# Kernel tuning notes

Hardware: AMD Instinct MI355X
Metric: run time of the kernel (lower is better)

## Reference

```python
import jax, jax.numpy as jnp
import numpy as np

IN_FEATURES = 1024
NUM_EXPERTS = 64
TOP_K = 2


def setup_inputs() -> dict:
    key = jax.random.key(0)
    kx, kw, kb = jax.random.split(key, 3)
    x = jax.random.normal(kx, (8, 4096, IN_FEATURES), dtype=jnp.float32)
    # nn.Linear init scale ~ 1/sqrt(in_features)
    bound = 1.0 / np.sqrt(IN_FEATURES)
    W = jax.random.uniform(kw, (NUM_EXPERTS, IN_FEATURES), dtype=jnp.float32, minval=-bound, maxval=bound)
    b = jax.random.uniform(kb, (NUM_EXPERTS,), dtype=jnp.float32, minval=-bound, maxval=bound)
    return {"x": x, "W": W, "b": b}


def reference(x, W, b):
    # logits: [B, S, E]
    logits = jnp.einsum("bsd,ed->bse", x, W) + b
    gates = jax.nn.softmax(logits, axis=-1)
    top_k_gates, top_k_indices = jax.lax.top_k(gates, TOP_K)
    return top_k_gates, top_k_indices
```

## Files before the change

### kernel.cpp

```cpp
#include <hip/hip_runtime.h>

#define D 1024
#define E 64
#define TPB 256
#define TOKS 64
#define NCH 8
#define CHB 32768

typedef __attribute__((ext_vector_type(8))) short bf16x8;
typedef __attribute__((ext_vector_type(8))) unsigned short u16x8;
typedef __attribute__((ext_vector_type(4))) float f32x4;
typedef __attribute__((ext_vector_type(4))) unsigned int u32x4;

__device__ __forceinline__ unsigned short bf16_rne(float f) {
    unsigned u = __builtin_bit_cast(unsigned, f);
    u += 0x7fffu + ((u >> 16) & 1u);
    return (unsigned short)(u >> 16);
}
__device__ __forceinline__ float bf16_to_f(unsigned short h) {
    unsigned u = ((unsigned)h) << 16;
    return __builtin_bit_cast(float, u);
}
__device__ __forceinline__ unsigned cvt_pk_bf16(float a, float b) {
    unsigned r;
    asm("v_cvt_pk_bf16_f32 %0, %1, %2" : "=v"(r) : "v"(a), "v"(b));
    return r;
}
__device__ __forceinline__ float lo_val(unsigned p) {
    return __builtin_bit_cast(float, p << 16);
}
__device__ __forceinline__ float hi_val(unsigned p) {
    return __builtin_bit_cast(float, p & 0xffff0000u);
}

__device__ __forceinline__ void split8_rne(f32x4 a, f32x4 b, bf16x8& hv, bf16x8& lv) {
    unsigned h0 = cvt_pk_bf16(a[0], a[1]);
    unsigned h1 = cvt_pk_bf16(a[2], a[3]);
    unsigned h2 = cvt_pk_bf16(b[0], b[1]);
    unsigned h3 = cvt_pk_bf16(b[2], b[3]);
    unsigned l0 = cvt_pk_bf16(a[0] - lo_val(h0), a[1] - hi_val(h0));
    unsigned l1 = cvt_pk_bf16(a[2] - lo_val(h1), a[3] - hi_val(h1));
    unsigned l2 = cvt_pk_bf16(b[0] - lo_val(h2), b[1] - hi_val(h2));
    unsigned l3 = cvt_pk_bf16(b[2] - lo_val(h3), b[3] - hi_val(h3));
    hv = __builtin_bit_cast(bf16x8, (u32x4){h0, h1, h2, h3});
    lv = __builtin_bit_cast(bf16x8, (u32x4){l0, l1, l2, l3});
}

__global__ __launch_bounds__(256) void router_prep(
        const float* __restrict__ W, unsigned short* __restrict__ Ws) {
    int t = blockIdx.x * 256 + threadIdx.x;
    int lane = t & 63;
    int nt = (t >> 6) & 3;
    int ks = t >> 8;
    int n = lane & 15, q = lane >> 4;
    const float* src = W + (size_t)(nt * 16 + n) * D + ks * 32 + q * 8;
    u16x8 hv, lv;
#pragma unroll
    for (int j = 0; j < 8; ++j) {
        float v = src[j];
        unsigned short h = bf16_rne(v);
        hv[j] = h;
        lv[j] = bf16_rne(v - bf16_to_f(h));
    }
    size_t base = ((size_t)(ks * 8 + nt * 2) * 64 + lane) * 8;
    *(u16x8*)(Ws + base)          = hv;
    *(u16x8*)(Ws + base + 64 * 8) = lv;
}

__global__ __launch_bounds__(TPB) void router_main(
        const float* __restrict__ x, const unsigned short* __restrict__ Ws,
        const float* __restrict__ bias, float* __restrict__ out, int T) {
    __shared__ __align__(16) union SM {
        unsigned char buf[2][CHB];
        float ls[TOKS][E + 1];
    } sm;
    __shared__ float sbias[E];

    const int tid  = threadIdx.x;
    const int lane = tid & 63;
    const int wid  = tid >> 6;
    const int n    = lane & 15;
    const int q    = lane >> 4;
    const int t0   = blockIdx.x * TOKS;

    if (tid < E) sbias[tid] = bias[tid];

    const float* arow = x + (size_t)(t0 + wid * 16 + n) * D + q * 8;
    const u32x4* gws  = (const u32x4*)Ws;

    f32x4 c0 = {0.f, 0.f, 0.f, 0.f}, c1 = c0, c2 = c0, c3 = c0;

    u32x4 W0, W1, W2, W3, W4, W5, W6, W7;
    f32x4 A0u, A0v, A1u, A1v, A2u, A2v, A3u, A3v;
    f32x4 N0u, N0v, N1u, N1v, N2u, N2v, N3u, N3v;

#define ISSUEW(c_) do {                                               \
        const u32x4* _g = gws + (size_t)(c_) * 2048 + tid;            \
        W0 = _g[0];    W1 = _g[256];  W2 = _g[512];  W3 = _g[768];    \
        W4 = _g[1024]; W5 = _g[1280]; W6 = _g[1536]; W7 = _g[1792];   \
    } while (0)

#define WRITEW(bi_) do {                                              \
        u32x4* _l = (u32x4*)sm.buf[bi_] + tid;                        \
        _l[0]    = W0; _l[256]  = W1; _l[512]  = W2; _l[768]  = W3;   \
        _l[1024] = W4; _l[1280] = W5; _l[1536] = W6; _l[1792] = W7;   \
    } while (0)

#define ISSUEA(p0u,p0v,p1u,p1v,p2u,p2v,p3u,p3v, c_) do {              \
        const float* _b = arow + (size_t)(c_) * 128;                  \
        p0u = *(const f32x4*)(_b);       p0v = *(const f32x4*)(_b + 4);   \
        p1u = *(const f32x4*)(_b + 32);  p1v = *(const f32x4*)(_b + 36);  \
        p2u = *(const f32x4*)(_b + 64);  p2v = *(const f32x4*)(_b + 68);  \
        p3u = *(const f32x4*)(_b + 96);  p3v = *(const f32x4*)(_b + 100); \
    } while (0)

#define MFMA __builtin_amdgcn_mfma_f32_16x16x32_bf16
#define COMPSTEP(bi_, ksl_, au_, av_) do {                            \
        bf16x8 ah, al;                                                \
        split8_rne(au_, av_, ah, al);                                 \
        const char* _p = (const char*)sm.buf[bi_] + (ksl_) * 8192 + lane * 16; \
        {                                                             \
            bf16x8 bh = *(const bf16x8*)(_p);                         \
            bf16x8 bl = *(const bf16x8*)(_p + 1024);                  \
            c0 = MFMA(ah, bh, c0, 0, 0, 0);                           \
            c0 = MFMA(al, bh, c0, 0, 0, 0);                           \
            c0 = MFMA(ah, bl, c0, 0, 0, 0);                           \
        }                                                             \
        {                                                             \
            bf16x8 bh = *(const bf16x8*)(_p + 2048);                  \
            bf16x8 bl = *(const bf16x8*)(_p + 3072);                  \
            c1 = MFMA(ah, bh, c1, 0, 0, 0);                           \
            c1 = MFMA(al, bh, c1, 0, 0, 0);                           \
            c1 = MFMA(ah, bl, c1, 0, 0, 0);                           \
        }                                                             \
        {                                                             \
            bf16x8 bh = *(const bf16x8*)(_p + 4096);                  \
            bf16x8 bl = *(const bf16x8*)(_p + 5120);                  \
            c2 = MFMA(ah, bh, c2, 0, 0, 0);                           \
            c2 = MFMA(al, bh, c2, 0, 0, 0);                           \
            c2 = MFMA(ah, bl, c2, 0, 0, 0);                           \
        }                                                             \
        {                                                             \
            bf16x8 bh = *(const bf16x8*)(_p + 6144);                  \
            bf16x8 bl = *(const bf16x8*)(_p + 7168);                  \
            c3 = MFMA(ah, bh, c3, 0, 0, 0);                           \
            c3 = MFMA(al, bh, c3, 0, 0, 0);                           \
            c3 = MFMA(ah, bl, c3, 0, 0, 0);                           \
        }                                                             \
    } while (0)

#define COMPCHUNK(bi_, p0u,p0v,p1u,p1v,p2u,p2v,p3u,p3v) do {          \
        COMPSTEP(bi_, 0, p0u, p0v);                                   \
        COMPSTEP(bi_, 1, p1u, p1v);                                   \
        COMPSTEP(bi_, 2, p2u, p2v);                                   \
        COMPSTEP(bi_, 3, p3u, p3v);                                   \
    } while (0)

    ISSUEW(0);
    ISSUEA(A0u,A0v,A1u,A1v,A2u,A2v,A3u,A3v, 0);
    WRITEW(0);
    __syncthreads();

    for (int c = 0; c < NCH; c += 2) {
        ISSUEW(c + 1);
        ISSUEA(N0u,N0v,N1u,N1v,N2u,N2v,N3u,N3v, c + 1);
        COMPCHUNK(0, A0u,A0v,A1u,A1v,A2u,A2v,A3u,A3v);
        WRITEW(1);
        __syncthreads();
        ISSUEW((c + 2) & (NCH - 1));
        ISSUEA(A0u,A0v,A1u,A1v,A2u,A2v,A3u,A3v, (c + 2) & (NCH - 1));
        COMPCHUNK(1, N0u,N0v,N1u,N1v,N2u,N2v,N3u,N3v);
        WRITEW(0);
        __syncthreads();
    }

    {
        const int row = wid * 16 + q * 4;
#define STORE_C(c_, nt_) do {                                         \
            int col = (nt_) * 16 + n;                                 \
            float bv = sbias[col];                                    \
            sm.ls[row + 0][col] = c_[0] + bv;                         \
            sm.ls[row + 1][col] = c_[1] + bv;                         \
            sm.ls[row + 2][col] = c_[2] + bv;                         \
            sm.ls[row + 3][col] = c_[3] + bv;                         \
        } while (0)
        STORE_C(c0, 0); STORE_C(c1, 1); STORE_C(c2, 2); STORE_C(c3, 3);
#undef STORE_C
    }
    __syncthreads();

    if (tid < TOKS) {
        float m1 = -3.4e38f, m2 = -3.4e38f;
        int i1 = 0, i2 = 0;
        for (int e = 0; e < E; ++e) {
            float v = sm.ls[tid][e];
            if (v > m1) { m2 = m1; i2 = i1; m1 = v; i1 = e; }
            else if (v > m2) { m2 = v; i2 = e; }
        }
        float Z = 0.f;
        for (int e = 0; e < E; ++e) Z += __expf(sm.ls[tid][e] - m1);
        float inv = 1.f / Z;
        int gt = t0 + tid;
        out[(size_t)gt * 2]     = inv;
        out[(size_t)gt * 2 + 1] = __expf(m2 - m1) * inv;
        float* oi = out + (size_t)T * 2;
        oi[(size_t)gt * 2]     = (float)i1;
        oi[(size_t)gt * 2 + 1] = (float)i2;
    }
}

extern "C" void kernel_launch(void* const* d_in, const int* in_sizes, int n_in,
                              void* d_out, int out_size, void* d_ws, size_t ws_size,
                              hipStream_t stream) {
    const float* x = (const float*)d_in[0];
    const float* W = (const float*)d_in[1];
    const float* b = (const float*)d_in[2];
    float* out = (float*)d_out;
    unsigned short* Ws = (unsigned short*)d_ws;
    int T = in_sizes[0] / D;
    hipLaunchKernelGGL(router_prep, dim3(32), dim3(256), 0, stream, W, Ws);
    hipLaunchKernelGGL(router_main, dim3(T / TOKS), dim3(TPB), 0, stream,
                       x, Ws, b, out, T);
}
```

Before: 204.0 us.

## Stage activation tiles through LDS with coalesced loads and halve chunk size

Activations were read straight from global memory per MFMA lane with strided 32-byte pieces. They are now loaded by rows of 16 contiguous float4s per token into a padded shared-memory tile, double-buffered alongside the weights, and read back in fragment layout. The chunk size drops from 128 to 64 K-elements (16 chunks), which cuts registers and LDS per stage but doubles the number of barriers. The goal is more coalesced global reads of x and lower register pressure, at the cost of extra LDS traffic and synchronisation.

```diff
diff --git a/kernel.cpp b/kernel.cpp
--- a/kernel.cpp
+++ b/kernel.cpp
@@ -4,8 +4,9 @@
 #define E 64
 #define TPB 256
 #define TOKS 64
-#define NCH 8
-#define CHB 32768
+#define NCH 16
+#define WCB 16384
+#define APITCH 68
 
 typedef __attribute__((ext_vector_type(8))) short bf16x8;
 typedef __attribute__((ext_vector_type(8))) unsigned short u16x8;
@@ -71,7 +72,10 @@
         const float* __restrict__ x, const unsigned short* __restrict__ Ws,
         const float* __restrict__ bias, float* __restrict__ out, int T) {
     __shared__ __align__(16) union SM {
-        unsigned char buf[2][CHB];
+        struct {
+            unsigned char w[2][WCB];
+            float a[2][TOKS][APITCH];
+        } k;
         float ls[TOKS][E + 1];
     } sm;
     __shared__ float sbias[E];
@@ -82,43 +86,46 @@
     const int n    = lane & 15;
     const int q    = lane >> 4;
     const int t0   = blockIdx.x * TOKS;
+    const int arow = tid >> 4;
+    const int acol = (tid & 15) * 4;
 
     if (tid < E) sbias[tid] = bias[tid];
 
-    const float* arow = x + (size_t)(t0 + wid * 16 + n) * D + q * 8;
-    const u32x4* gws  = (const u32x4*)Ws;
+    const float* xb = x + (size_t)t0 * D + acol;
+    const u32x4* gws = (const u32x4*)Ws;
 
     f32x4 c0 = {0.f, 0.f, 0.f, 0.f}, c1 = c0, c2 = c0, c3 = c0;
 
-    u32x4 W0, W1, W2, W3, W4, W5, W6, W7;
-    f32x4 A0u, A0v, A1u, A1v, A2u, A2v, A3u, A3v;
-    f32x4 N0u, N0v, N1u, N1v, N2u, N2v, N3u, N3v;
-
-#define ISSUEW(c_) do {                                               \
-        const u32x4* _g = gws + (size_t)(c_) * 2048 + tid;            \
-        W0 = _g[0];    W1 = _g[256];  W2 = _g[512];  W3 = _g[768];    \
-        W4 = _g[1024]; W5 = _g[1280]; W6 = _g[1536]; W7 = _g[1792];   \
+    u32x4 W0, W1, W2, W3;
+    f32x4 A0, A1, A2, A3;
+
+#define ISSUE(c_) do {                                                \
+        const u32x4* _g = gws + (size_t)(c_) * 1024 + tid;            \
+        W0 = _g[0]; W1 = _g[256]; W2 = _g[512]; W3 = _g[768];         \
+        const float* _x = xb + (c_) * 64;                             \
+        A0 = *(const f32x4*)(_x + (size_t)(arow     ) * D);           \
+        A1 = *(const f32x4*)(_x + (size_t)(arow + 16) * D);           \
+        A2 = *(const f32x4*)(_x + (size_t)(arow + 32) * D);           \
+        A3 = *(const f32x4*)(_x + (size_t)(arow + 48) * D);           \
     } while (0)
 
-#define WRITEW(bi_) do {                                              \
-        u32x4* _l = (u32x4*)sm.buf[bi_] + tid;                        \
-        _l[0]    = W0; _l[256]  = W1; _l[512]  = W2; _l[768]  = W3;   \
-        _l[1024] = W4; _l[1280] = W5; _l[1536] = W6; _l[1792] = W7;   \
+#define WRITE(bi_) do {                                               \
+        u32x4* _l = (u32x4*)sm.k.w[bi_] + tid;                        \
+        _l[0] = W0; _l[256] = W1; _l[512] = W2; _l[768] = W3;         \
+        *(f32x4*)&sm.k.a[bi_][arow     ][acol] = A0;                  \
+        *(f32x4*)&sm.k.a[bi_][arow + 16][acol] = A1;                  \
+        *(f32x4*)&sm.k.a[bi_][arow + 32][acol] = A2;                  \
+        *(f32x4*)&sm.k.a[bi_][arow + 48][acol] = A3;                  \
     } while (0)
 
-#define ISSUEA(p0u,p0v,p1u,p1v,p2u,p2v,p3u,p3v, c_) do {              \
-        const float* _b = arow + (size_t)(c_) * 128;                  \
-        p0u = *(const f32x4*)(_b);       p0v = *(const f32x4*)(_b + 4);   \
-        p1u = *(const f32x4*)(_b + 32);  p1v = *(const f32x4*)(_b + 36);  \
-        p2u = *(const f32x4*)(_b + 64);  p2v = *(const f32x4*)(_b + 68);  \
-        p3u = *(const f32x4*)(_b + 96);  p3v = *(const f32x4*)(_b + 100); \
-    } while (0)
-
 #define MFMA __builtin_amdgcn_mfma_f32_16x16x32_bf16
-#define COMPSTEP(bi_, ksl_, au_, av_) do {                            \
+#define COMPSTEP(bi_, ksl_) do {                                      \
+        const float* _a = &sm.k.a[bi_][wid * 16 + n][(ksl_) * 32 + q * 8]; \
+        f32x4 au = *(const f32x4*)_a;                                 \
+        f32x4 av = *(const f32x4*)(_a + 4);                           \
         bf16x8 ah, al;                                                \
-        split8_rne(au_, av_, ah, al);                                 \
-        const char* _p = (const char*)sm.buf[bi_] + (ksl_) * 8192 + lane * 16; \
+        split8_rne(au, av, ah, al);                                   \
+        const char* _p = (const char*)sm.k.w[bi_] + (ksl_) * 8192 + lane * 16; \
         {                                                             \
             bf16x8 bh = *(const bf16x8*)(_p);                         \
             bf16x8 bl = *(const bf16x8*)(_p + 1024);                  \
@@ -149,28 +156,20 @@
         }                                                             \
     } while (0)
 
-#define COMPCHUNK(bi_, p0u,p0v,p1u,p1v,p2u,p2v,p3u,p3v) do {          \
-        COMPSTEP(bi_, 0, p0u, p0v);                                   \
-        COMPSTEP(bi_, 1, p1u, p1v);                                   \
-        COMPSTEP(bi_, 2, p2u, p2v);                                   \
-        COMPSTEP(bi_, 3, p3u, p3v);                                   \
-    } while (0)
-
-    ISSUEW(0);
-    ISSUEA(A0u,A0v,A1u,A1v,A2u,A2v,A3u,A3v, 0);
-    WRITEW(0);
+    ISSUE(0);
+    WRITE(0);
     __syncthreads();
 
     for (int c = 0; c < NCH; c += 2) {
-        ISSUEW(c + 1);
-        ISSUEA(N0u,N0v,N1u,N1v,N2u,N2v,N3u,N3v, c + 1);
-        COMPCHUNK(0, A0u,A0v,A1u,A1v,A2u,A2v,A3u,A3v);
-        WRITEW(1);
+        ISSUE(c + 1);
+        COMPSTEP(0, 0);
+        COMPSTEP(0, 1);
+        WRITE(1);
         __syncthreads();
-        ISSUEW((c + 2) & (NCH - 1));
-        ISSUEA(A0u,A0v,A1u,A1v,A2u,A2v,A3u,A3v, (c + 2) & (NCH - 1));
-        COMPCHUNK(1, N0u,N0v,N1u,N1v,N2u,N2v,N3u,N3v);
-        WRITEW(0);
+        ISSUE((c + 2) & (NCH - 1));
+        COMPSTEP(1, 0);
+        COMPSTEP(1, 1);
+        WRITE(0);
         __syncthreads();
     }
 
```

Result: slower. 208.4 us (+2.2%).
